# Optimization experiments

Measured on AMD Instinct MI355X. Metric: run time of the kernel, lower is better.

The kernel has to match this reference:

```python
import jax, jax.numpy as jnp
import numpy as np

B, TOPN, OUT, PAD, IOU_TH, IM = 16, 4, 224, 224, 0.25, 448
HP = IM + 2 * PAD  # padded image side = 896

_ANCHOR_SETTINGS = (
    dict(stride=32, size=48, scale=[2 ** (1. / 3.), 2 ** (2. / 3.)], aspect_ratio=[0.667, 1, 1.5]),
    dict(stride=64, size=96, scale=[2 ** (1. / 3.), 2 ** (2. / 3.)], aspect_ratio=[0.667, 1, 1.5]),
    dict(stride=128, size=192, scale=[1, 2 ** (1. / 3.), 2 ** (2. / 3.)], aspect_ratio=[0.667, 1, 1.5]),
)

def _edge_anchors(input_shape=(IM, IM)):
    # NTS-Net generate_default_anchor_maps: per layer, loop scale then aspect,
    # each emitting an HxW map flattened row-major -> matches tidy conv channel-major flatten.
    out = []
    for a in _ANCHOR_SETTINGS:
        st = a['stride']
        H = int(np.ceil(input_shape[0] / st)); W = int(np.ceil(input_shape[1] / st))
        cy = np.broadcast_to((np.arange(H) * st + st / 2.)[:, None], (H, W))
        cx = np.broadcast_to((np.arange(W) * st + st / 2.)[None, :], (H, W))
        for sc in a['scale']:
            for ar in a['aspect_ratio']:
                h = a['size'] * sc / np.sqrt(ar); w = a['size'] * sc * np.sqrt(ar)
                out.append(np.stack([cy - h / 2., cx - w / 2., cy + h / 2., cx + w / 2.], -1).reshape(-1, 4))
    e = np.concatenate(out, 0)
    return (e + PAD).astype(np.int32)  # module does (edge_anchors + 224).astype(int)


def _conv(x, w, b, stride, pad):
    y = jax.lax.conv_general_dilated(x, w, (stride, stride), [(pad, pad), (pad, pad)],
                                     dimension_numbers=('NCHW', 'OIHW', 'NCHW'))
    return y + b[None, :, None, None]


def _proposal_scores(rpn, w1, b1, w2, b2, w3, b3, wt1, bt1, wt2, bt2, wt3, bt3):
    d1 = jax.nn.relu(_conv(rpn, w1, b1, 1, 1))   # [B,128,14,14]
    d2 = jax.nn.relu(_conv(d1, w2, b2, 2, 1))    # [B,128,7,7]
    d3 = jax.nn.relu(_conv(d2, w3, b3, 2, 1))    # [B,128,4,4]
    bsz = rpn.shape[0]
    t1 = _conv(d1, wt1, bt1, 1, 0).reshape(bsz, -1)  # [B,1176]
    t2 = _conv(d2, wt2, bt2, 1, 0).reshape(bsz, -1)  # [B,294]
    t3 = _conv(d3, wt3, bt3, 1, 0).reshape(bsz, -1)  # [B,144]
    return jnp.concatenate([t1, t2, t3], axis=1)     # [B,1614]


def _nms_topn(scores, boxes, areas):
    # greedy hard NMS, fixed TOPN picks, suppress iou >= IOU_TH (matches upstream hard_nms)
    def step(s, _):
        i = jnp.argmax(s)
        sb = boxes[i]
        iy = jnp.clip(jnp.minimum(boxes[:, 2], sb[2]) - jnp.maximum(boxes[:, 0], sb[0]), 0.)
        ix = jnp.clip(jnp.minimum(boxes[:, 3], sb[3]) - jnp.maximum(boxes[:, 1], sb[1]), 0.)
        inter = iy * ix
        iou = inter / (areas + areas[i] - inter)
        return jnp.where(iou >= IOU_TH, -jnp.inf, s), i
    _, idxs = jax.lax.scan(step, scores, None, length=TOPN)
    return idxs  # [TOPN] int


def _crop_resize(x, anchors, top_idx):
    # batched replacement of the per-(i,j) F.interpolate(x_pad[i,:,y0:y1,x0:x1], 224, bilinear, align_corners=True)
    x_pad = jnp.pad(x, ((0, 0), (0, 0), (PAD, PAD), (PAD, PAD)))
    xp = jnp.transpose(x_pad, (0, 2, 3, 1))            # [B,HP,HP,3]
    bxs = anchors[top_idx].astype(jnp.float32)          # [B,T,4] (y0,x0,y1,x1)
    y0, x0, y1, x1 = bxs[..., 0], bxs[..., 1], bxs[..., 2], bxs[..., 3]
    t = jnp.arange(OUT, dtype=jnp.float32) / (OUT - 1)  # align_corners=True grid
    ys = y0[..., None] + t * (y1 - y0 - 1.)[..., None]  # [B,T,S] src rows in padded img
    xs = x0[..., None] + t * (x1 - x0 - 1.)[..., None]
    yi0 = jnp.floor(ys).astype(jnp.int32); yi1 = jnp.minimum(yi0 + 1, HP - 1)
    xi0 = jnp.floor(xs).astype(jnp.int32); xi1 = jnp.minimum(xi0 + 1, HP - 1)
    wy = (ys - yi0)[..., :, None, None]                 # [B,T,S,1,1]
    wx = (xs - xi0)[..., None, :, None]                 # [B,T,1,S,1]
    b = jnp.arange(x.shape[0])[:, None, None, None]
    g = lambda yi, xi: xp[b, yi[..., :, None], xi[..., None, :]]  # [B,T,S,S,3]
    v = (g(yi0, xi0) * (1 - wy) * (1 - wx) + g(yi0, xi1) * (1 - wy) * wx
         + g(yi1, xi0) * wy * (1 - wx) + g(yi1, xi1) * wy * wx)
    return jnp.transpose(v, (0, 1, 4, 2, 3))            # [B,T,3,S,S]


def setup_inputs() -> dict:
    key = jax.random.key(0)
    ks = jax.random.split(key, 16)
    he = lambda k, shape, fan: jax.random.normal(k, shape, jnp.float32) * np.sqrt(2.0 / fan)
    inp = {
        'x': jax.random.normal(ks[0], (B, 3, IM, IM), jnp.float32),
        'rpn_feature': jax.random.uniform(ks[1], (B, 2048, 14, 14), jnp.float32),
        'w_down1': he(ks[2], (128, 2048, 3, 3), 2048 * 9), 'b_down1': jnp.zeros((128,), jnp.float32),
        'w_down2': he(ks[3], (128, 128, 3, 3), 128 * 9),   'b_down2': jnp.zeros((128,), jnp.float32),
        'w_down3': he(ks[4], (128, 128, 3, 3), 128 * 9),   'b_down3': jnp.zeros((128,), jnp.float32),
        'w_tidy1': he(ks[5], (6, 128, 1, 1), 128),         'b_tidy1': jnp.zeros((6,), jnp.float32),
        'w_tidy2': he(ks[6], (6, 128, 1, 1), 128),         'b_tidy2': jnp.zeros((6,), jnp.float32),
        'w_tidy3': he(ks[7], (9, 128, 1, 1), 128),         'b_tidy3': jnp.zeros((9,), jnp.float32),
        'anchors': jnp.asarray(_edge_anchors(), jnp.int32),  # [1614,4]
    }
    return inp


def reference(x, rpn_feature, w_down1, b_down1, w_down2, b_down2, w_down3, b_down3,
              w_tidy1, b_tidy1, w_tidy2, b_tidy2, w_tidy3, b_tidy3, anchors):
    rpn_score = _proposal_scores(rpn_feature, w_down1, b_down1, w_down2, b_down2, w_down3, b_down3,
                                 w_tidy1, b_tidy1, w_tidy2, b_tidy2, w_tidy3, b_tidy3)
    boxes = anchors.astype(jnp.float32)
    areas = (boxes[:, 2] - boxes[:, 0]) * (boxes[:, 3] - boxes[:, 1])
    top_idx = jax.vmap(lambda s: _nms_topn(s, boxes, areas))(rpn_score)       # [B,TOPN]
    top_prob = jnp.take_along_axis(rpn_score, top_idx, axis=1)                # [B,TOPN]
    part_imgs = _crop_resize(x, anchors, top_idx).reshape(B * TOPN, 3, OUT, OUT)
    return part_imgs, top_idx, top_prob, rpn_score
```

## Files before the change

### kernel.cpp

```cpp
#include <hip/hip_runtime.h>
#include <math.h>

#define BATCH 16
#define TOPN 4
#define OUTS 224
#define PADW 224
#define IM 448
#define HP 896
#define NA 1614
#define IC1 2048
#define C128 128

#define N_PART (BATCH*TOPN*3*OUTS*OUTS)
#define OFF_TOPIDX  (N_PART)
#define OFF_TOPPROB (N_PART + BATCH*TOPN)
#define OFF_SCORE   (N_PART + 2*BATCH*TOPN)

#define WS_D1 0
#define WS_IDX (BATCH*C128*196)
#define WS_WT  (WS_IDX + 64)
#define NWT1 (9*2048*128)
#define NWT2 (9*128*128)
#define NIMG (16*32*16384)
#define D1SL 25088

typedef __attribute__((ext_vector_type(8))) short frag8;
typedef __attribute__((ext_vector_type(16))) float acc16;
typedef __attribute__((ext_vector_type(4)))  float acc4;

__device__ __forceinline__ unsigned short f2bf(float f) {
    unsigned int u = __float_as_uint(f);
    u = (u + 0x7fffu + ((u >> 16) & 1u)) >> 16;
    return (unsigned short)u;
}
__device__ __forceinline__ float bf2f(unsigned short h) {
    return __uint_as_float(((unsigned int)h) << 16);
}
__device__ __forceinline__ void cvt4(const float* v, ushort4* h, ushort4* lo) {
    unsigned short hh[4], ll[4];
#pragma unroll
    for (int e = 0; e < 4; ++e) { hh[e] = f2bf(v[e]); ll[e] = f2bf(v[e] - bf2f(hh[e])); }
    *h  = make_ushort4(hh[0], hh[1], hh[2], hh[3]);
    *lo = make_ushort4(ll[0], ll[1], ll[2], ll[3]);
}

__device__ __forceinline__ void w1frag_body(const float* __restrict__ w1,
                                            unsigned short* __restrict__ w1h,
                                            unsigned short* __restrict__ w1l,
                                            int i) {
    if (i >= 32768) return;
    int oc5 = i & 31;
    int q8  = (i >> 5) & 1;
    int ot  = (i >> 6) & 3;
    int c   = (i >> 8) & 3;
    int h   = (i >> 10) & 1;
    int kg  = (i >> 11) & 15;
    int oc  = ot * 32 + oc5;
    int ic0 = kg * 128 + h * 64 + c * 16 + q8 * 8;
    int l   = q8 * 32 + oc5;
    const float* src = w1 + ((size_t)oc * IC1 + ic0) * 9;
    size_t dbase = (size_t)kg * 16384 + h * 8192 + c * 2048 + ot * 512 + l * 8;
#pragma unroll
    for (int t = 0; t < 9; ++t) {
        frag8 hv, lv;
#pragma unroll
        for (int e = 0; e < 8; ++e) {
            float v = src[e * 9 + t];
            unsigned short hs = f2bf(v);
            hv[e] = (short)hs;
            lv[e] = (short)f2bf(v - bf2f(hs));
        }
        size_t dst = dbase + (size_t)t * 262144;
        *(frag8*)&w1h[dst] = hv;
        *(frag8*)&w1l[dst] = lv;
    }
}

__device__ __forceinline__ void wfrag128_body(const float* __restrict__ w,
                                              unsigned short* __restrict__ wh,
                                              unsigned short* __restrict__ wl,
                                              int i) {
    if (i >= 16384) return;
    int oc5 = i & 31;
    int q8  = (i >> 5) & 1;
    int ot  = (i >> 6) & 3;
    int c   = (i >> 8) & 3;
    int h   = (i >> 10) & 1;
    int oc  = ot * 32 + oc5;
    int ic0 = h * 64 + c * 16 + q8 * 8;
    int l   = q8 * 32 + oc5;
    const float* src = w + ((size_t)oc * C128 + ic0) * 9;
    size_t dbase = (size_t)h * 8192 + c * 2048 + ot * 512 + l * 8;
#pragma unroll
    for (int t = 0; t < 9; ++t) {
        frag8 hv, lv;
#pragma unroll
        for (int e = 0; e < 8; ++e) {
            float v = src[e * 9 + t];
            unsigned short hs = f2bf(v);
            hv[e] = (short)hs;
            lv[e] = (short)f2bf(v - bf2f(hs));
        }
        size_t dst = dbase + (size_t)t * 16384;
        *(frag8*)&wh[dst] = hv;
        *(frag8*)&wl[dst] = lv;
    }
}

__global__ __launch_bounds__(256) void k_prep(
    const float* __restrict__ w1, unsigned short* __restrict__ w1h, unsigned short* __restrict__ w1l,
    const float* __restrict__ w2, unsigned short* __restrict__ w2fh, unsigned short* __restrict__ w2fl,
    const float* __restrict__ w3, unsigned short* __restrict__ w3fh, unsigned short* __restrict__ w3fl,
    const float* __restrict__ rpn, unsigned short* __restrict__ imgH) {
    __shared__ float tile[64 * 201];
    const int tid = threadIdx.x;
    const int blk = blockIdx.x;
    if (blk < 128) {
        w1frag_body(w1, w1h, w1l, blk * 256 + tid);
    } else if (blk < 192) {
        wfrag128_body(w2, w2fh, w2fl, (blk - 128) * 256 + tid);
    } else if (blk < 256) {
        wfrag128_body(w3, w3fh, w3fl, (blk - 192) * 256 + tid);
    } else {
        const int bb = blk - 256;
        const int b = bb & 15, icg = bb >> 4;
        const int ic0 = icg * 64;
        char* img = (char*)(imgH + (size_t)bb * 16384);
        for (int qq = tid; qq < 3136; qq += 256) {
            int icl = qq / 49, r = qq % 49, p = r * 4;
            const float4 v = *(const float4*)&rpn[(size_t)(b * IC1 + ic0 + icl) * 196 + p];
            tile[icl * 201 + p + 0] = v.x;
            tile[icl * 201 + p + 1] = v.y;
            tile[icl * 201 + p + 2] = v.z;
            tile[icl * 201 + p + 3] = v.w;
        }
        __syncthreads();
        for (int qq = tid; qq < 3136; qq += 256) {
            int px = qq >> 4, ic4 = (qq & 15) * 4;
            float vv[4];
            unsigned short hh[4];
#pragma unroll
            for (int e = 0; e < 4; ++e) { vv[e] = tile[(ic4 + e) * 201 + px]; hh[e] = f2bf(vv[e]); }
            int pos = (px / 14 + 1) * 16 + (px % 14 + 1);
            int byo = (pos * 128 + ic4 * 2) ^ ((pos & 7) << 4);
            *(ushort4*)(img + byo) = make_ushort4(hh[0], hh[1], hh[2], hh[3]);
        }
        for (int qq = tid; qq < 960; qq += 256) {
            int hp = qq >> 4, sub = qq & 15;
            int pos;
            if (hp < 16)      pos = hp;
            else if (hp < 32) pos = 240 + (hp - 16);
            else if (hp < 46) pos = (hp - 31) * 16;
            else              pos = (hp - 45) * 16 + 15;
            *(ushort4*)(img + pos * 128 + sub * 8) = make_ushort4(0, 0, 0, 0);
        }
    }
}


#define LOADB(it, BH, BL) { \
    const int o_ = ((it) >> 2) * 262144 + ((it) & 3) * 2048; \
    BH = *(const frag8*)&WHb[o_]; BL = *(const frag8*)&WLb[o_]; }

#define DOMFMA(it, BH, BL) { \
    const int tap_ = (it) >> 2; \
    const int off_ = (tap_ / 3) * 16 + (tap_ % 3); \
    const int kb_ = ((it) & 3) * 32 + q * 16; \
    frag8 aH[4]; \
    _Pragma("unroll") \
    for (int mt_ = 0; mt_ < 4; ++mt_) { \
        const int p_ = posa[mt_] + off_; \
        const int by_ = (p_ * 128 + kb_) ^ ((p_ & 7) << 4); \
        aH[mt_] = *(const frag8*)((const char*)inH + by_); \
    } \
    _Pragma("unroll") \
    for (int mt_ = 0; mt_ < 4; ++mt_) { \
        acc[mt_] = __builtin_amdgcn_mfma_f32_32x32x16_bf16(aH[mt_], BH, acc[mt_], 0, 0, 0); \
        acc[mt_] = __builtin_amdgcn_mfma_f32_32x32x16_bf16(aH[mt_], BL, acc[mt_], 0, 0, 0); \
    } }

__global__ __launch_bounds__(512, 4) void k_conv1_mfma(const unsigned short* __restrict__ imgH,
                                                       const unsigned short* __restrict__ wfh,
                                                       const unsigned short* __restrict__ wfl,
                                                       float* __restrict__ d1p) {
    __shared__ unsigned short inH[256 * 64];

    const int tid = threadIdx.x;
    const int blk = blockIdx.x;
    const int b = blk >> 5;
    const int icg = blk & 31;
    const int l = tid & 63, w = tid >> 6;
    const int ln = l & 31, q = l >> 5;
    const int mtw = w & 1, ntw = w >> 1;

    {
        const char* src = (const char*)(imgH + ((size_t)(icg * 16 + b)) * 16384);
        char* dst = (char*)inH;
#pragma unroll
        for (int k = 0; k < 4; ++k) {
            frag8 v = *(const frag8*)(src + tid * 16 + k * 8192);
            *(frag8*)(dst + tid * 16 + k * 8192) = v;
        }
    }

    acc16 acc[4];
#pragma unroll
    for (int mt = 0; mt < 4; ++mt)
#pragma unroll
        for (int r = 0; r < 16; ++r) acc[mt][r] = 0.f;

    int posa[4];
#pragma unroll
    for (int mt = 0; mt < 4; ++mt) {
        int px = mtw * 128 + mt * 32 + ln;
        posa[mt] = (px < 196) ? ((px / 14) * 16 + (px % 14)) : 0;
    }

    const unsigned short* WHb = wfh + (size_t)icg * 8192 + ntw * 512 + (size_t)l * 8;
    const unsigned short* WLb = wfl + (size_t)icg * 8192 + ntw * 512 + (size_t)l * 8;

    __syncthreads();

    frag8 B0H, B0L, B1H, B1L, B2H, B2L;
    LOADB(0, B0H, B0L);
    LOADB(1, B1H, B1L);
    LOADB(2, B2H, B2L);
#pragma unroll
    for (int g = 0; g < 12; ++g) {
        DOMFMA(g * 3 + 0, B0H, B0L); if (g < 11) LOADB(g * 3 + 3, B0H, B0L);
        DOMFMA(g * 3 + 1, B1H, B1L); if (g < 11) LOADB(g * 3 + 4, B1H, B1L);
        DOMFMA(g * 3 + 2, B2H, B2L); if (g < 11) LOADB(g * 3 + 5, B2H, B2L);
    }

    {
        float* out = d1p + (size_t)blk * D1SL;
        const int oc = ntw * 32 + ln;
#pragma unroll
        for (int mt = 0; mt < 4; ++mt) {
#pragma unroll
            for (int r = 0; r < 16; ++r) {
                int m = (r & 3) + 8 * (r >> 2) + 4 * q;
                int px = mtw * 128 + mt * 32 + m;
                if (px < 196)
                    out[px * 128 + oc] = acc[mt][r];
            }
        }
    }
}

__global__ __launch_bounds__(256) void k_reduce(const float* __restrict__ d1p,
                                                const float* __restrict__ b1,
                                                float* __restrict__ d1) {
    int f4 = blockIdx.x * 256 + threadIdx.x;
    int flat = f4 * 4;
    int b = flat / D1SL;
    int inner = flat - b * D1SL;
    const float* src = d1p + (size_t)b * 32 * D1SL + inner;
    float4 s = *(const float4*)&b1[inner & 127];
#pragma unroll 8
    for (int icg = 0; icg < 32; ++icg) {
        float4 v = *(const float4*)&src[(size_t)icg * D1SL];
        s.x += v.x; s.y += v.y; s.z += v.z; s.w += v.w;
    }
    s.x = fmaxf(s.x, 0.f); s.y = fmaxf(s.y, 0.f);
    s.z = fmaxf(s.z, 0.f); s.w = fmaxf(s.w, 0.f);
    *(float4*)&d1[flat] = s;
}


#define LOADB2(it, BH, BL) { \
    const int o_ = ((it) >> 2) * 16384 + ((it) & 3) * 2048; \
    BH = *(const frag8*)&W2H[o_]; BL = *(const frag8*)&W2L[o_]; }

#define DOC2(it, BH, BL) { \
    const int tap_ = (it) >> 2; \
    const int off_ = (tap_ / 3) * 16 + (tap_ % 3); \
    const int ko_ = ((it) & 3) * 16 + q * 8; \
    const int pp_ = (posa2 + off_) * 72 + ko_; \
    frag8 aH = *(const frag8*)&inH[pp_]; \
    frag8 aL = *(const frag8*)&inL[pp_]; \
    c2 = __builtin_amdgcn_mfma_f32_32x32x16_bf16(aH, BH, c2, 0, 0, 0); \
    c2 = __builtin_amdgcn_mfma_f32_32x32x16_bf16(aH, BL, c2, 0, 0, 0); \
    c2 = __builtin_amdgcn_mfma_f32_32x32x16_bf16(aL, BH, c2, 0, 0, 0); }

#define LOADB3(it, BH, BL) { \
    const int o_ = ((it) >> 2) * 16384 + ((it) & 3) * 2048; \
    BH = *(const frag8*)&W3Hp[o_]; BL = *(const frag8*)&W3Lp[o_]; }

#define DOC3(it, BH, BL) { \
    const int tap_ = (it) >> 2; \
    const int off_ = (tap_ / 3) * 16 + (tap_ % 3); \
    const int ko_ = ((it) & 3) * 16 + q * 8; \
    const int pp_ = (posb3 + off_) * 72 + ko_; \
    frag8 aH = *(const frag8*)&dhH[pp_]; \
    frag8 aL = *(const frag8*)&dhL[pp_]; \
    c3 = __builtin_amdgcn_mfma_f32_32x32x16_bf16(aH, BH, c3, 0, 0, 0); \
    c3 = __builtin_amdgcn_mfma_f32_32x32x16_bf16(aH, BL, c3, 0, 0, 0); \
    c3 = __builtin_amdgcn_mfma_f32_32x32x16_bf16(aL, BH, c3, 0, 0, 0); }

__global__ __launch_bounds__(512, 1) void k_tail(
    const float* __restrict__ d1,
    const unsigned short* __restrict__ w2fh, const unsigned short* __restrict__ w2fl,
    const unsigned short* __restrict__ w3fh, const unsigned short* __restrict__ w3fl,
    const float* __restrict__ b2, const float* __restrict__ b3,
    const float* __restrict__ wt1, const float* __restrict__ bt1,
    const float* __restrict__ wt2, const float* __restrict__ bt2,
    const float* __restrict__ wt3, const float* __restrict__ bt3,
    const int* __restrict__ anchors,
    float* __restrict__ score_out, float* __restrict__ out_idx,
    float* __restrict__ out_prob, int* __restrict__ idx_ws) {
    extern __shared__ char smem[];
    unsigned short* inH = (unsigned short*)(smem);
    unsigned short* inL = (unsigned short*)(smem + 43776);
    unsigned short* t1H = (unsigned short*)(smem + 124416);
    unsigned short* t1L = (unsigned short*)(smem + 126720);
    float*  d2f  = (float*)(smem + 129024);
    float*  sbuf = (float*)(smem + 154112);
    unsigned short* dhH = (unsigned short*)(smem);
    unsigned short* dhL = (unsigned short*)(smem + 27648);
    float*  d3f  = (float*)(smem + 55296);
    unsigned short* t2H = (unsigned short*)(smem + 63488);
    unsigned short* t2L = (unsigned short*)(smem + 65792);
    float* wt3s = (float*)(smem);
    float* y0s = (float*)(smem + 6464);
    float* x0s = (float*)(smem + 12928);
    float* y1s = (float*)(smem + 19392);
    float* x1s = (float*)(smem + 25856);
    float* ars = (float*)(smem + 32320);
    float* rv  = (float*)(smem + 38784);
    int*   ri  = (int*)(smem + 39808);

    const int tid = threadIdx.x;
    const int b = blockIdx.x;
    const int l = tid & 63, w = tid >> 6;
    const int ln = l & 31, q = l >> 5;
    const int l16 = l & 15, q4 = l >> 4;

    for (int i = tid; i < 304 * 72; i += 512) { inH[i] = 0; inL[i] = 0; }

    acc16 c2;
    acc4 t1a[2];
#pragma unroll
    for (int r = 0; r < 16; ++r) c2[r] = 0.f;
#pragma unroll
    for (int i = 0; i < 2; ++i)
#pragma unroll
        for (int r = 0; r < 4; ++r) t1a[i][r] = 0.f;

    const int mtw = w & 1, ntw = w >> 1;
    int posa2;
    {
        int px = mtw * 32 + ln;
        posa2 = (px < 49) ? ((px / 7) * 32 + (px % 7) * 2) : 256;
    }
    __syncthreads();

    for (int half = 0; half < 2; ++half) {
        const int ics = half * 64;
        for (int qq = tid; qq < 3136; qq += 512) {
            int px = qq >> 4, ic4 = (qq & 15) * 4;
            float4 v = *(const float4*)&d1[(size_t)(b * 196 + px) * 128 + ics + ic4];
            float vv[4] = {fmaxf(v.x, 0.f), fmaxf(v.y, 0.f), fmaxf(v.z, 0.f), fmaxf(v.w, 0.f)};
            ushort4 h4, l4; cvt4(vv, &h4, &l4);
            int pos = (px / 14 + 1) * 16 + (px % 14 + 1);
            *(ushort4*)&inH[pos * 72 + ic4] = h4;
            *(ushort4*)&inL[pos * 72 + ic4] = l4;
        }
        for (int qq = tid; qq < 1024; qq += 512) {
            int m = qq >> 6, k = qq & 63;
            float v = (m < 6) ? wt1[m * 128 + ics + k] : 0.f;
            unsigned short h = f2bf(v);
            t1H[m * 72 + k] = h;
            t1L[m * 72 + k] = f2bf(v - bf2f(h));
        }
        __syncthreads();

        {
            const unsigned short* W2H = w2fh + half * 8192 + ntw * 512 + (size_t)l * 8;
            const unsigned short* W2L = w2fl + half * 8192 + ntw * 512 + (size_t)l * 8;
            frag8 B0H, B0L, B1H, B1L, B2H, B2L, B3H, B3L;
            LOADB2(0, B0H, B0L);
            LOADB2(1, B1H, B1L);
            LOADB2(2, B2H, B2L);
            LOADB2(3, B3H, B3L);
#pragma unroll
            for (int g = 0; g < 9; ++g) {
                DOC2(g * 4 + 0, B0H, B0L); if (g < 8) LOADB2(g * 4 + 4, B0H, B0L);
                DOC2(g * 4 + 1, B1H, B1L); if (g < 8) LOADB2(g * 4 + 5, B1H, B1L);
                DOC2(g * 4 + 2, B2H, B2L); if (g < 8) LOADB2(g * 4 + 6, B2H, B2L);
                DOC2(g * 4 + 3, B3H, B3L); if (g < 8) LOADB2(g * 4 + 7, B3H, B3L);
            }
        }

#pragma unroll
        for (int i = 0; i < 2; ++i) {
            int px = (w * 2 + i) * 16 + l16;
            int pos = (px < 196) ? ((px / 14 + 1) * 16 + (px % 14 + 1)) : 256;
#pragma unroll
            for (int c = 0; c < 2; ++c) {
                int ko = c * 32 + q4 * 8;
                frag8 aH = *(const frag8*)&t1H[l16 * 72 + ko];
                frag8 aL = *(const frag8*)&t1L[l16 * 72 + ko];
                frag8 bH = *(const frag8*)&inH[pos * 72 + ko];
                frag8 bL = *(const frag8*)&inL[pos * 72 + ko];
                t1a[i] = __builtin_amdgcn_mfma_f32_16x16x32_bf16(aH, bH, t1a[i], 0, 0, 0);
                t1a[i] = __builtin_amdgcn_mfma_f32_16x16x32_bf16(aH, bL, t1a[i], 0, 0, 0);
                t1a[i] = __builtin_amdgcn_mfma_f32_16x16x32_bf16(aL, bH, t1a[i], 0, 0, 0);
            }
        }
        __syncthreads();
    }

    {
        int oc = ntw * 32 + ln;
        float bias = b2[oc];
#pragma unroll
        for (int r = 0; r < 16; ++r) {
            int m = (r & 3) + 8 * (r >> 2) + 4 * q;
            int px = mtw * 32 + m;
            if (px < 49) d2f[px * 128 + oc] = fmaxf(c2[r] + bias, 0.f);
        }
    }
#pragma unroll
    for (int i = 0; i < 2; ++i) {
        int px = (w * 2 + i) * 16 + l16;
#pragma unroll
        for (int r = 0; r < 4; ++r) {
            int oc = q4 * 4 + r;
            if (oc < 6 && px < 196) {
                float v = t1a[i][r] + bt1[oc];
                sbuf[oc * 196 + px] = v;
                score_out[b * NA + oc * 196 + px] = v;
            }
        }
    }
    __syncthreads();

    for (int i = tid; i < 192 * 72; i += 512) { dhH[i] = 0; dhL[i] = 0; }

    acc16 c3;
    acc4 t2a;
#pragma unroll
    for (int r = 0; r < 16; ++r) c3[r] = 0.f;
#pragma unroll
    for (int r = 0; r < 4; ++r) t2a[r] = 0.f;

    const int posb3 = (ln < 16) ? ((ln / 4) * 32 + (ln % 4) * 2) : 144;
    const int pxt2 = (w - 4) * 16 + l16;
    const int posbt2 = (w >= 4 && pxt2 < 49) ? ((pxt2 / 7 + 1) * 16 + (pxt2 % 7 + 1)) : 144;
    __syncthreads();

    for (int half = 0; half < 2; ++half) {
        const int ics = half * 64;
        for (int qq = tid; qq < 784; qq += 512) {
            int px = qq >> 4, ic4 = (qq & 15) * 4;
            float4 v = *(const float4*)&d2f[px * 128 + ics + ic4];
            float vv[4] = {v.x, v.y, v.z, v.w};
            ushort4 h4, l4; cvt4(vv, &h4, &l4);
            int pos = (px / 7 + 1) * 16 + (px % 7 + 1);
            *(ushort4*)&dhH[pos * 72 + ic4] = h4;
            *(ushort4*)&dhL[pos * 72 + ic4] = l4;
        }
        for (int qq = tid; qq < 1024; qq += 512) {
            int m = qq >> 6, k = qq & 63;
            float v = (m < 6) ? wt2[m * 128 + ics + k] : 0.f;
            unsigned short h = f2bf(v);
            t2H[m * 72 + k] = h;
            t2L[m * 72 + k] = f2bf(v - bf2f(h));
        }
        __syncthreads();

        if (w < 4) {
            const unsigned short* W3Hp = w3fh + half * 8192 + w * 512 + (size_t)l * 8;
            const unsigned short* W3Lp = w3fl + half * 8192 + w * 512 + (size_t)l * 8;
            frag8 B0H, B0L, B1H, B1L, B2H, B2L, B3H, B3L;
            LOADB3(0, B0H, B0L);
            LOADB3(1, B1H, B1L);
            LOADB3(2, B2H, B2L);
            LOADB3(3, B3H, B3L);
#pragma unroll
            for (int g = 0; g < 9; ++g) {
                DOC3(g * 4 + 0, B0H, B0L); if (g < 8) LOADB3(g * 4 + 4, B0H, B0L);
                DOC3(g * 4 + 1, B1H, B1L); if (g < 8) LOADB3(g * 4 + 5, B1H, B1L);
                DOC3(g * 4 + 2, B2H, B2L); if (g < 8) LOADB3(g * 4 + 6, B2H, B2L);
                DOC3(g * 4 + 3, B3H, B3L); if (g < 8) LOADB3(g * 4 + 7, B3H, B3L);
            }
        } else {
#pragma unroll
            for (int c = 0; c < 2; ++c) {
                int ko = c * 32 + q4 * 8;
                frag8 aH = *(const frag8*)&t2H[l16 * 72 + ko];
                frag8 aL = *(const frag8*)&t2L[l16 * 72 + ko];
                frag8 bH = *(const frag8*)&dhH[posbt2 * 72 + ko];
                frag8 bL = *(const frag8*)&dhL[posbt2 * 72 + ko];
                t2a = __builtin_amdgcn_mfma_f32_16x16x32_bf16(aH, bH, t2a, 0, 0, 0);
                t2a = __builtin_amdgcn_mfma_f32_16x16x32_bf16(aH, bL, t2a, 0, 0, 0);
                t2a = __builtin_amdgcn_mfma_f32_16x16x32_bf16(aL, bH, t2a, 0, 0, 0);
            }
        }
        __syncthreads();
    }

    if (w < 4) {
        int oc = w * 32 + ln;
        float bias = b3[oc];
#pragma unroll
        for (int r = 0; r < 16; ++r) {
            int px = (r & 3) + 8 * (r >> 2) + 4 * q;
            if (px < 16) d3f[oc * 16 + px] = fmaxf(c3[r] + bias, 0.f);
        }
    } else {
#pragma unroll
        for (int r = 0; r < 4; ++r) {
            int oc = q4 * 4 + r;
            if (oc < 6 && pxt2 < 49) {
                float v = t2a[r] + bt2[oc];
                sbuf[1176 + oc * 49 + pxt2] = v;
                score_out[b * NA + 1176 + oc * 49 + pxt2] = v;
            }
        }
    }
    for (int i = tid; i < 1152; i += 512) wt3s[i] = wt3[i];
    __syncthreads();

    if (tid < 144) {
        int oc = tid >> 4, px = tid & 15;
        float s = bt3[oc];
        for (int ic = 0; ic < 128; ++ic) s += wt3s[oc * 128 + ic] * d3f[ic * 16 + px];
        sbuf[1470 + oc * 16 + px] = s;
        score_out[b * NA + 1470 + oc * 16 + px] = s;
    }
    for (int j = tid; j < NA; j += 512) {
        int4 a = ((const int4*)anchors)[j];
        float a0 = (float)a.x, a1 = (float)a.y, a2 = (float)a.z, a3 = (float)a.w;
        y0s[j] = a0; x0s[j] = a1; y1s[j] = a2; x1s[j] = a3;
        ars[j] = (a2 - a0) * (a3 - a1);
    }
    __syncthreads();

    for (int it = 0; it < TOPN; ++it) {
        float bv = -INFINITY; int bi = NA;
        for (int j = tid; j < NA; j += 512) {
            float v = sbuf[j];
            if (v > bv || (v == bv && j < bi)) { bv = v; bi = j; }
        }
#pragma unroll
        for (int d = 1; d < 64; d <<= 1) {
            float ov = __shfl_xor(bv, d, 64);
            int   oi = __shfl_xor(bi, d, 64);
            if (ov > bv || (ov == bv && oi < bi)) { bv = ov; bi = oi; }
        }
        if (l == 0) { rv[w] = bv; ri[w] = bi; }
        __syncthreads();
        if (tid == 0) {
            float V = rv[0]; int K = ri[0];
#pragma unroll
            for (int j = 1; j < 8; ++j) {
                float ov = rv[j]; int oi = ri[j];
                if (ov > V || (ov == V && oi < K)) { V = ov; K = oi; }
            }
            ri[8] = K;
            out_idx[b * TOPN + it] = (float)K;
            out_prob[b * TOPN + it] = V;
            idx_ws[b * TOPN + it] = K;
        }
        __syncthreads();
        int K = ri[8];
        float ky0 = y0s[K], kx0 = x0s[K], ky1 = y1s[K], kx1 = x1s[K], ka = ars[K];
        for (int j = tid; j < NA; j += 512) {
            float iy = fmaxf(fminf(y1s[j], ky1) - fmaxf(y0s[j], ky0), 0.f);
            float ix = fmaxf(fminf(x1s[j], kx1) - fmaxf(x0s[j], kx0), 0.f);
            float inter = iy * ix;
            float iou = inter / (ars[j] + ka - inter);
            if (iou >= 0.25f) sbuf[j] = -INFINITY;
        }
        __syncthreads();
    }
}

__global__ __launch_bounds__(256) void k_crop(const float* __restrict__ x,
                                              const int* __restrict__ anchors,
                                              const int* __restrict__ idx_ws,
                                              float* __restrict__ out) {
    int blk = blockIdx.x;
    int crop = blk / OUTS;
    int i = blk % OUTS;
    int j = threadIdx.x;
    if (j >= OUTS) return;
    int b = crop >> 2;
    int a = idx_ws[crop];
    int y0 = anchors[a * 4], x0 = anchors[a * 4 + 1];
    int y1 = anchors[a * 4 + 2], x1 = anchors[a * 4 + 3];

    float ti = (float)i / 223.f;
    float ys = (float)y0 + ti * (float)(y1 - y0 - 1);
    int yi0 = (int)ys;
    int yi1 = min(yi0 + 1, HP - 1);
    float wy = ys - (float)yi0;

    float tj = (float)j / 223.f;
    float xs = (float)x0 + tj * (float)(x1 - x0 - 1);
    int xi0 = (int)xs;
    int xi1 = min(xi0 + 1, HP - 1);
    float wx = xs - (float)xi0;

    int ry0 = yi0 - PADW, ry1 = yi1 - PADW, rx0 = xi0 - PADW, rx1 = xi1 - PADW;
    bool vy0 = (ry0 >= 0) && (ry0 < IM), vy1 = (ry1 >= 0) && (ry1 < IM);
    bool vx0 = (rx0 >= 0) && (rx0 < IM), vx1 = (rx1 >= 0) && (rx1 < IM);

    float w00 = (1.f - wy) * (1.f - wx), w01 = (1.f - wy) * wx;
    float w10 = wy * (1.f - wx), w11 = wy * wx;

#pragma unroll
    for (int c = 0; c < 3; ++c) {
        const float* xp = x + (size_t)(b * 3 + c) * IM * IM;
        float g00 = (vy0 && vx0) ? xp[ry0 * IM + rx0] : 0.f;
        float g01 = (vy0 && vx1) ? xp[ry0 * IM + rx1] : 0.f;
        float g10 = (vy1 && vx0) ? xp[ry1 * IM + rx0] : 0.f;
        float g11 = (vy1 && vx1) ? xp[ry1 * IM + rx1] : 0.f;
        out[(size_t)(crop * 3 + c) * OUTS * OUTS + i * OUTS + j] =
            g00 * w00 + g01 * w01 + g10 * w10 + g11 * w11;
    }
}

extern "C" void kernel_launch(void* const* d_in, const int* in_sizes, int n_in,
                              void* d_out, int out_size, void* d_ws, size_t ws_size,
                              hipStream_t stream) {
    (void)in_sizes; (void)n_in; (void)out_size; (void)ws_size;
    const float* x    = (const float*)d_in[0];
    const float* rpn  = (const float*)d_in[1];
    const float* w1   = (const float*)d_in[2];
    const float* b1   = (const float*)d_in[3];
    const float* w2   = (const float*)d_in[4];
    const float* b2   = (const float*)d_in[5];
    const float* w3   = (const float*)d_in[6];
    const float* b3   = (const float*)d_in[7];
    const float* wt1  = (const float*)d_in[8];
    const float* bt1  = (const float*)d_in[9];
    const float* wt2  = (const float*)d_in[10];
    const float* bt2  = (const float*)d_in[11];
    const float* wt3  = (const float*)d_in[12];
    const float* bt3  = (const float*)d_in[13];
    const int*   anc  = (const int*)d_in[14];

    float* out = (float*)d_out;
    float* ws  = (float*)d_ws;
    float* d1  = ws + WS_D1;
    int*   idxw = (int*)(ws + WS_IDX);
    unsigned short* w1h = (unsigned short*)(ws + WS_WT);
    unsigned short* w1l = w1h + NWT1;
    unsigned short* w2fh = w1l + NWT1;
    unsigned short* w2fl = w2fh + NWT2;
    unsigned short* w3fh = w2fl + NWT2;
    unsigned short* w3fl = w3fh + NWT2;
    unsigned short* imgH = w3fl + NWT2;
    float* d1p = (float*)(imgH + NIMG);

    static const int TAIL_LDS = 160568;
    hipFuncSetAttribute((const void*)k_tail, hipFuncAttributeMaxDynamicSharedMemorySize, TAIL_LDS);

    k_prep<<<768, 256, 0, stream>>>(w1, w1h, w1l, w2, w2fh, w2fl, w3, w3fh, w3fl,
                                    rpn, imgH);
    k_conv1_mfma<<<512, 512, 0, stream>>>(imgH, w1h, w1l, d1p);
    k_reduce<<<392, 256, 0, stream>>>(d1p, b1, d1);
    k_tail<<<BATCH, 512, TAIL_LDS, stream>>>(d1, w2fh, w2fl, w3fh, w3fl, b2, b3,
                                             wt1, bt1, wt2, bt2, wt3, bt3, anc,
                                             out + OFF_SCORE, out + OFF_TOPIDX,
                                             out + OFF_TOPPROB, idxw);
    k_crop<<<BATCH * TOPN * OUTS, 256, 0, stream>>>(x, anc, idxw, out);
}
```

Measured before the change: 261.8 us.

## Split tail kernel into conv2, conv3 and NMS kernels with split-K across warps

The single 16-block tail kernel (one block per batch) is split into three kernels. Conv2 and conv3 now run on 128 and 64 blocks that tile over output channels and pixels. Inside each block the four warps split the reduction over channels and combine partial sums through shared memory. Intermediate activations d2/d3 and the scores now go through global memory, and there are two extra kernel launches. The aim is to use far more compute units for the tail, at the cost of the extra global traffic, launch overhead and redundant input staging per block.

```diff
diff --git a/kernel.cpp b/kernel.cpp
--- a/kernel.cpp
+++ b/kernel.cpp
@@ -157,7 +157,6 @@
     }
 }
 
-
 #define LOADB(it, BH, BL) { \
     const int o_ = ((it) >> 2) * 262144 + ((it) & 3) * 2048; \
     BH = *(const frag8*)&WHb[o_]; BL = *(const frag8*)&WLb[o_]; }
@@ -267,77 +266,27 @@
     *(float4*)&d1[flat] = s;
 }
 
-
-#define LOADB2(it, BH, BL) { \
-    const int o_ = ((it) >> 2) * 16384 + ((it) & 3) * 2048; \
-    BH = *(const frag8*)&W2H[o_]; BL = *(const frag8*)&W2L[o_]; }
-
-#define DOC2(it, BH, BL) { \
-    const int tap_ = (it) >> 2; \
-    const int off_ = (tap_ / 3) * 16 + (tap_ % 3); \
-    const int ko_ = ((it) & 3) * 16 + q * 8; \
-    const int pp_ = (posa2 + off_) * 72 + ko_; \
-    frag8 aH = *(const frag8*)&inH[pp_]; \
-    frag8 aL = *(const frag8*)&inL[pp_]; \
-    c2 = __builtin_amdgcn_mfma_f32_32x32x16_bf16(aH, BH, c2, 0, 0, 0); \
-    c2 = __builtin_amdgcn_mfma_f32_32x32x16_bf16(aH, BL, c2, 0, 0, 0); \
-    c2 = __builtin_amdgcn_mfma_f32_32x32x16_bf16(aL, BH, c2, 0, 0, 0); }
-
-#define LOADB3(it, BH, BL) { \
-    const int o_ = ((it) >> 2) * 16384 + ((it) & 3) * 2048; \
-    BH = *(const frag8*)&W3Hp[o_]; BL = *(const frag8*)&W3Lp[o_]; }
-
-#define DOC3(it, BH, BL) { \
-    const int tap_ = (it) >> 2; \
-    const int off_ = (tap_ / 3) * 16 + (tap_ % 3); \
-    const int ko_ = ((it) & 3) * 16 + q * 8; \
-    const int pp_ = (posb3 + off_) * 72 + ko_; \
-    frag8 aH = *(const frag8*)&dhH[pp_]; \
-    frag8 aL = *(const frag8*)&dhL[pp_]; \
-    c3 = __builtin_amdgcn_mfma_f32_32x32x16_bf16(aH, BH, c3, 0, 0, 0); \
-    c3 = __builtin_amdgcn_mfma_f32_32x32x16_bf16(aH, BL, c3, 0, 0, 0); \
-    c3 = __builtin_amdgcn_mfma_f32_32x32x16_bf16(aL, BH, c3, 0, 0, 0); }
-
-__global__ __launch_bounds__(512, 1) void k_tail(
+__global__ __launch_bounds__(256, 1) void k_conv2t1(
     const float* __restrict__ d1,
     const unsigned short* __restrict__ w2fh, const unsigned short* __restrict__ w2fl,
-    const unsigned short* __restrict__ w3fh, const unsigned short* __restrict__ w3fl,
-    const float* __restrict__ b2, const float* __restrict__ b3,
+    const float* __restrict__ b2,
     const float* __restrict__ wt1, const float* __restrict__ bt1,
-    const float* __restrict__ wt2, const float* __restrict__ bt2,
-    const float* __restrict__ wt3, const float* __restrict__ bt3,
-    const int* __restrict__ anchors,
-    float* __restrict__ score_out, float* __restrict__ out_idx,
-    float* __restrict__ out_prob, int* __restrict__ idx_ws) {
-    extern __shared__ char smem[];
-    unsigned short* inH = (unsigned short*)(smem);
-    unsigned short* inL = (unsigned short*)(smem + 43776);
-    unsigned short* t1H = (unsigned short*)(smem + 124416);
-    unsigned short* t1L = (unsigned short*)(smem + 126720);
-    float*  d2f  = (float*)(smem + 129024);
-    float*  sbuf = (float*)(smem + 154112);
-    unsigned short* dhH = (unsigned short*)(smem);
-    unsigned short* dhL = (unsigned short*)(smem + 27648);
-    float*  d3f  = (float*)(smem + 55296);
-    unsigned short* t2H = (unsigned short*)(smem + 63488);
-    unsigned short* t2L = (unsigned short*)(smem + 65792);
-    float* wt3s = (float*)(smem);
-    float* y0s = (float*)(smem + 6464);
-    float* x0s = (float*)(smem + 12928);
-    float* y1s = (float*)(smem + 19392);
-    float* x1s = (float*)(smem + 25856);
-    float* ars = (float*)(smem + 32320);
-    float* rv  = (float*)(smem + 38784);
-    int*   ri  = (int*)(smem + 39808);
+    float* __restrict__ d2, float* __restrict__ score_out) {
+    __shared__ unsigned short inH[304 * 72];
+    __shared__ unsigned short inL[304 * 72];
+    __shared__ unsigned short t1H[16 * 72];
+    __shared__ unsigned short t1L[16 * 72];
+    __shared__ float red[3 * 64 * 16];
 
     const int tid = threadIdx.x;
-    const int b = blockIdx.x;
+    const int blk = blockIdx.x;
+    const int b = blk >> 3;
+    const int pt = (blk >> 2) & 1;
+    const int ot = blk & 3;
     const int l = tid & 63, w = tid >> 6;
     const int ln = l & 31, q = l >> 5;
     const int l16 = l & 15, q4 = l >> 4;
 
-    for (int i = tid; i < 304 * 72; i += 512) { inH[i] = 0; inL[i] = 0; }
-
     acc16 c2;
     acc4 t1a[2];
 #pragma unroll
@@ -347,17 +296,19 @@
 #pragma unroll
         for (int r = 0; r < 4; ++r) t1a[i][r] = 0.f;
 
-    const int mtw = w & 1, ntw = w >> 1;
     int posa2;
     {
-        int px = mtw * 32 + ln;
+        int px = pt * 32 + ln;
         posa2 = (px < 49) ? ((px / 7) * 32 + (px % 7) * 2) : 256;
     }
+    const int ko = w * 16 + q * 8;
+
+    for (int i = tid; i < 304 * 72; i += 256) { inH[i] = 0; inL[i] = 0; }
     __syncthreads();
 
     for (int half = 0; half < 2; ++half) {
         const int ics = half * 64;
-        for (int qq = tid; qq < 3136; qq += 512) {
+        for (int qq = tid; qq < 3136; qq += 256) {
             int px = qq >> 4, ic4 = (qq & 15) * 4;
             float4 v = *(const float4*)&d1[(size_t)(b * 196 + px) * 128 + ics + ic4];
             float vv[4] = {fmaxf(v.x, 0.f), fmaxf(v.y, 0.f), fmaxf(v.z, 0.f), fmaxf(v.w, 0.f)};
@@ -366,77 +317,110 @@
             *(ushort4*)&inH[pos * 72 + ic4] = h4;
             *(ushort4*)&inL[pos * 72 + ic4] = l4;
         }
-        for (int qq = tid; qq < 1024; qq += 512) {
-            int m = qq >> 6, k = qq & 63;
-            float v = (m < 6) ? wt1[m * 128 + ics + k] : 0.f;
-            unsigned short h = f2bf(v);
-            t1H[m * 72 + k] = h;
-            t1L[m * 72 + k] = f2bf(v - bf2f(h));
+        if (ot == 0) {
+            for (int qq = tid; qq < 1024; qq += 256) {
+                int m = qq >> 6, k = qq & 63;
+                float v = (m < 6) ? wt1[m * 128 + ics + k] : 0.f;
+                unsigned short h = f2bf(v);
+                t1H[m * 72 + k] = h;
+                t1L[m * 72 + k] = f2bf(v - bf2f(h));
+            }
         }
         __syncthreads();
 
         {
-            const unsigned short* W2H = w2fh + half * 8192 + ntw * 512 + (size_t)l * 8;
-            const unsigned short* W2L = w2fl + half * 8192 + ntw * 512 + (size_t)l * 8;
-            frag8 B0H, B0L, B1H, B1L, B2H, B2L, B3H, B3L;
-            LOADB2(0, B0H, B0L);
-            LOADB2(1, B1H, B1L);
-            LOADB2(2, B2H, B2L);
-            LOADB2(3, B3H, B3L);
-#pragma unroll
-            for (int g = 0; g < 9; ++g) {
-                DOC2(g * 4 + 0, B0H, B0L); if (g < 8) LOADB2(g * 4 + 4, B0H, B0L);
-                DOC2(g * 4 + 1, B1H, B1L); if (g < 8) LOADB2(g * 4 + 5, B1H, B1L);
-                DOC2(g * 4 + 2, B2H, B2L); if (g < 8) LOADB2(g * 4 + 6, B2H, B2L);
-                DOC2(g * 4 + 3, B3H, B3L); if (g < 8) LOADB2(g * 4 + 7, B3H, B3L);
-            }
-        }
-
+            const unsigned short* W2B  = w2fh + half * 8192 + w * 2048 + ot * 512 + (size_t)l * 8;
+            const unsigned short* W2Bl = w2fl + half * 8192 + w * 2048 + ot * 512 + (size_t)l * 8;
+            frag8 B0H = *(const frag8*)&W2B[0],     B0L = *(const frag8*)&W2Bl[0];
+            frag8 B1H = *(const frag8*)&W2B[16384], B1L = *(const frag8*)&W2Bl[16384];
+#pragma unroll
+            for (int j = 0; j < 9; ++j) {
+                const int off = (j / 3) * 16 + (j % 3);
+                const int pp = (posa2 + off) * 72 + ko;
+                frag8 aH = *(const frag8*)&inH[pp];
+                frag8 aL = *(const frag8*)&inL[pp];
+                frag8 BH = (j & 1) ? B1H : B0H;
+                frag8 BL = (j & 1) ? B1L : B0L;
+                c2 = __builtin_amdgcn_mfma_f32_32x32x16_bf16(aH, BH, c2, 0, 0, 0);
+                c2 = __builtin_amdgcn_mfma_f32_32x32x16_bf16(aH, BL, c2, 0, 0, 0);
+                c2 = __builtin_amdgcn_mfma_f32_32x32x16_bf16(aL, BH, c2, 0, 0, 0);
+                if (j < 7) {
+                    if (j & 1) { B1H = *(const frag8*)&W2B[(j + 2) * 16384]; B1L = *(const frag8*)&W2Bl[(j + 2) * 16384]; }
+                    else       { B0H = *(const frag8*)&W2B[(j + 2) * 16384]; B0L = *(const frag8*)&W2Bl[(j + 2) * 16384]; }
+                }
+            }
+        }
+
+        if (ot == 0) {
+#pragma unroll
+            for (int i = 0; i < 2; ++i) {
+                int px = (pt * 8 + w * 2 + i) * 16 + l16;
+                int pos = (px < 196) ? ((px / 14 + 1) * 16 + (px % 14 + 1)) : 256;
+#pragma unroll
+                for (int c = 0; c < 2; ++c) {
+                    int kot = c * 32 + q4 * 8;
+                    frag8 aH = *(const frag8*)&t1H[l16 * 72 + kot];
+                    frag8 aL = *(const frag8*)&t1L[l16 * 72 + kot];
+                    frag8 bH = *(const frag8*)&inH[pos * 72 + kot];
+                    frag8 bL = *(const frag8*)&inL[pos * 72 + kot];
+                    t1a[i] = __builtin_amdgcn_mfma_f32_16x16x32_bf16(aH, bH, t1a[i], 0, 0, 0);
+                    t1a[i] = __builtin_amdgcn_mfma_f32_16x16x32_bf16(aH, bL, t1a[i], 0, 0, 0);
+                    t1a[i] = __builtin_amdgcn_mfma_f32_16x16x32_bf16(aL, bH, t1a[i], 0, 0, 0);
+                }
+            }
+        }
+        __syncthreads();
+    }
+
+    if (w > 0) {
+#pragma unroll
+        for (int r = 0; r < 16; ++r) red[((w - 1) * 64 + l) * 16 + r] = c2[r];
+    }
+    __syncthreads();
+    if (w == 0) {
+        const int oc = ot * 32 + ln;
+        float bias = b2[oc];
+#pragma unroll
+        for (int r = 0; r < 16; ++r) {
+            float s = c2[r] + red[(0 * 64 + l) * 16 + r] + red[(1 * 64 + l) * 16 + r] + red[(2 * 64 + l) * 16 + r];
+            int m = (r & 3) + 8 * (r >> 2) + 4 * q;
+            int px = pt * 32 + m;
+            if (px < 49) d2[(size_t)(b * 49 + px) * 128 + oc] = fmaxf(s + bias, 0.f);
+        }
+    }
+    if (ot == 0) {
 #pragma unroll
         for (int i = 0; i < 2; ++i) {
-            int px = (w * 2 + i) * 16 + l16;
-            int pos = (px < 196) ? ((px / 14 + 1) * 16 + (px % 14 + 1)) : 256;
-#pragma unroll
-            for (int c = 0; c < 2; ++c) {
-                int ko = c * 32 + q4 * 8;
-                frag8 aH = *(const frag8*)&t1H[l16 * 72 + ko];
-                frag8 aL = *(const frag8*)&t1L[l16 * 72 + ko];
-                frag8 bH = *(const frag8*)&inH[pos * 72 + ko];
-                frag8 bL = *(const frag8*)&inL[pos * 72 + ko];
-                t1a[i] = __builtin_amdgcn_mfma_f32_16x16x32_bf16(aH, bH, t1a[i], 0, 0, 0);
-                t1a[i] = __builtin_amdgcn_mfma_f32_16x16x32_bf16(aH, bL, t1a[i], 0, 0, 0);
-                t1a[i] = __builtin_amdgcn_mfma_f32_16x16x32_bf16(aL, bH, t1a[i], 0, 0, 0);
-            }
-        }
-        __syncthreads();
-    }
-
-    {
-        int oc = ntw * 32 + ln;
-        float bias = b2[oc];
-#pragma unroll
-        for (int r = 0; r < 16; ++r) {
-            int m = (r & 3) + 8 * (r >> 2) + 4 * q;
-            int px = mtw * 32 + m;
-            if (px < 49) d2f[px * 128 + oc] = fmaxf(c2[r] + bias, 0.f);
-        }
-    }
-#pragma unroll
-    for (int i = 0; i < 2; ++i) {
-        int px = (w * 2 + i) * 16 + l16;
-#pragma unroll
-        for (int r = 0; r < 4; ++r) {
-            int oc = q4 * 4 + r;
-            if (oc < 6 && px < 196) {
-                float v = t1a[i][r] + bt1[oc];
-                sbuf[oc * 196 + px] = v;
-                score_out[b * NA + oc * 196 + px] = v;
-            }
-        }
-    }
-    __syncthreads();
-
-    for (int i = tid; i < 192 * 72; i += 512) { dhH[i] = 0; dhL[i] = 0; }
+            int px = (pt * 8 + w * 2 + i) * 16 + l16;
+#pragma unroll
+            for (int r = 0; r < 4; ++r) {
+                int oc = q4 * 4 + r;
+                if (oc < 6 && px < 196)
+                    score_out[b * NA + oc * 196 + px] = t1a[i][r] + bt1[oc];
+            }
+        }
+    }
+}
+
+__global__ __launch_bounds__(256, 1) void k_conv3t2(
+    const float* __restrict__ d2,
+    const unsigned short* __restrict__ w3fh, const unsigned short* __restrict__ w3fl,
+    const float* __restrict__ b3,
+    const float* __restrict__ wt2, const float* __restrict__ bt2,
+    float* __restrict__ d3, float* __restrict__ score_out) {
+    __shared__ unsigned short dhH[192 * 72];
+    __shared__ unsigned short dhL[192 * 72];
+    __shared__ unsigned short t2H[16 * 72];
+    __shared__ unsigned short t2L[16 * 72];
+    __shared__ float red[3 * 64 * 16];
+
+    const int tid = threadIdx.x;
+    const int blk = blockIdx.x;
+    const int b = blk >> 2;
+    const int ot = blk & 3;
+    const int l = tid & 63, w = tid >> 6;
+    const int ln = l & 31, q = l >> 5;
+    const int l16 = l & 15, q4 = l >> 4;
 
     acc16 c3;
     acc4 t2a;
@@ -446,53 +430,66 @@
     for (int r = 0; r < 4; ++r) t2a[r] = 0.f;
 
     const int posb3 = (ln < 16) ? ((ln / 4) * 32 + (ln % 4) * 2) : 144;
-    const int pxt2 = (w - 4) * 16 + l16;
-    const int posbt2 = (w >= 4 && pxt2 < 49) ? ((pxt2 / 7 + 1) * 16 + (pxt2 % 7 + 1)) : 144;
+    const int pxt2 = w * 16 + l16;
+    const int posbt2 = (pxt2 < 49) ? ((pxt2 / 7 + 1) * 16 + (pxt2 % 7 + 1)) : 144;
+    const int ko = w * 16 + q * 8;
+
+    for (int i = tid; i < 192 * 72; i += 256) { dhH[i] = 0; dhL[i] = 0; }
     __syncthreads();
 
     for (int half = 0; half < 2; ++half) {
         const int ics = half * 64;
-        for (int qq = tid; qq < 784; qq += 512) {
+        for (int qq = tid; qq < 784; qq += 256) {
             int px = qq >> 4, ic4 = (qq & 15) * 4;
-            float4 v = *(const float4*)&d2f[px * 128 + ics + ic4];
+            float4 v = *(const float4*)&d2[(size_t)(b * 49 + px) * 128 + ics + ic4];
             float vv[4] = {v.x, v.y, v.z, v.w};
             ushort4 h4, l4; cvt4(vv, &h4, &l4);
             int pos = (px / 7 + 1) * 16 + (px % 7 + 1);
             *(ushort4*)&dhH[pos * 72 + ic4] = h4;
             *(ushort4*)&dhL[pos * 72 + ic4] = l4;
         }
-        for (int qq = tid; qq < 1024; qq += 512) {
-            int m = qq >> 6, k = qq & 63;
-            float v = (m < 6) ? wt2[m * 128 + ics + k] : 0.f;
-            unsigned short h = f2bf(v);
-            t2H[m * 72 + k] = h;
-            t2L[m * 72 + k] = f2bf(v - bf2f(h));
-        }
-        __syncthreads();
-
-        if (w < 4) {
-            const unsigned short* W3Hp = w3fh + half * 8192 + w * 512 + (size_t)l * 8;
-            const unsigned short* W3Lp = w3fl + half * 8192 + w * 512 + (size_t)l * 8;
-            frag8 B0H, B0L, B1H, B1L, B2H, B2L, B3H, B3L;
-            LOADB3(0, B0H, B0L);
-            LOADB3(1, B1H, B1L);
-            LOADB3(2, B2H, B2L);
-            LOADB3(3, B3H, B3L);
-#pragma unroll
-            for (int g = 0; g < 9; ++g) {
-                DOC3(g * 4 + 0, B0H, B0L); if (g < 8) LOADB3(g * 4 + 4, B0H, B0L);
-                DOC3(g * 4 + 1, B1H, B1L); if (g < 8) LOADB3(g * 4 + 5, B1H, B1L);
-                DOC3(g * 4 + 2, B2H, B2L); if (g < 8) LOADB3(g * 4 + 6, B2H, B2L);
-                DOC3(g * 4 + 3, B3H, B3L); if (g < 8) LOADB3(g * 4 + 7, B3H, B3L);
-            }
-        } else {
+        if (ot == 0) {
+            for (int qq = tid; qq < 1024; qq += 256) {
+                int m = qq >> 6, k = qq & 63;
+                float v = (m < 6) ? wt2[m * 128 + ics + k] : 0.f;
+                unsigned short h = f2bf(v);
+                t2H[m * 72 + k] = h;
+                t2L[m * 72 + k] = f2bf(v - bf2f(h));
+            }
+        }
+        __syncthreads();
+
+        {
+            const unsigned short* W3B  = w3fh + half * 8192 + w * 2048 + ot * 512 + (size_t)l * 8;
+            const unsigned short* W3Bl = w3fl + half * 8192 + w * 2048 + ot * 512 + (size_t)l * 8;
+            frag8 B0H = *(const frag8*)&W3B[0],     B0L = *(const frag8*)&W3Bl[0];
+            frag8 B1H = *(const frag8*)&W3B[16384], B1L = *(const frag8*)&W3Bl[16384];
+#pragma unroll
+            for (int j = 0; j < 9; ++j) {
+                const int off = (j / 3) * 16 + (j % 3);
+                const int pp = (posb3 + off) * 72 + ko;
+                frag8 aH = *(const frag8*)&dhH[pp];
+                frag8 aL = *(const frag8*)&dhL[pp];
+                frag8 BH = (j & 1) ? B1H : B0H;
+                frag8 BL = (j & 1) ? B1L : B0L;
+                c3 = __builtin_amdgcn_mfma_f32_32x32x16_bf16(aH, BH, c3, 0, 0, 0);
+                c3 = __builtin_amdgcn_mfma_f32_32x32x16_bf16(aH, BL, c3, 0, 0, 0);
+                c3 = __builtin_amdgcn_mfma_f32_32x32x16_bf16(aL, BH, c3, 0, 0, 0);
+                if (j < 7) {
+                    if (j & 1) { B1H = *(const frag8*)&W3B[(j + 2) * 16384]; B1L = *(const frag8*)&W3Bl[(j + 2) * 16384]; }
+                    else       { B0H = *(const frag8*)&W3B[(j + 2) * 16384]; B0L = *(const frag8*)&W3Bl[(j + 2) * 16384]; }
+                }
+            }
+        }
+
+        if (ot == 0) {
 #pragma unroll
             for (int c = 0; c < 2; ++c) {
-                int ko = c * 32 + q4 * 8;
-                frag8 aH = *(const frag8*)&t2H[l16 * 72 + ko];
-                frag8 aL = *(const frag8*)&t2L[l16 * 72 + ko];
-                frag8 bH = *(const frag8*)&dhH[posbt2 * 72 + ko];
-                frag8 bL = *(const frag8*)&dhL[posbt2 * 72 + ko];
+                int kot = c * 32 + q4 * 8;
+                frag8 aH = *(const frag8*)&t2H[l16 * 72 + kot];
+                frag8 aL = *(const frag8*)&t2L[l16 * 72 + kot];
+                frag8 bH = *(const frag8*)&dhH[posbt2 * 72 + kot];
+                frag8 bL = *(const frag8*)&dhL[posbt2 * 72 + kot];
                 t2a = __builtin_amdgcn_mfma_f32_16x16x32_bf16(aH, bH, t2a, 0, 0, 0);
                 t2a = __builtin_amdgcn_mfma_f32_16x16x32_bf16(aH, bL, t2a, 0, 0, 0);
                 t2a = __builtin_amdgcn_mfma_f32_16x16x32_bf16(aL, bH, t2a, 0, 0, 0);
@@ -501,40 +498,63 @@
         __syncthreads();
     }
 
-    if (w < 4) {
-        int oc = w * 32 + ln;
+    if (w > 0) {
+#pragma unroll
+        for (int r = 0; r < 16; ++r) red[((w - 1) * 64 + l) * 16 + r] = c3[r];
+    }
+    __syncthreads();
+    if (w == 0) {
+        const int oc = ot * 32 + ln;
         float bias = b3[oc];
 #pragma unroll
         for (int r = 0; r < 16; ++r) {
+            float s = c3[r] + red[(0 * 64 + l) * 16 + r] + red[(1 * 64 + l) * 16 + r] + red[(2 * 64 + l) * 16 + r];
             int px = (r & 3) + 8 * (r >> 2) + 4 * q;
-            if (px < 16) d3f[oc * 16 + px] = fmaxf(c3[r] + bias, 0.f);
-        }
-    } else {
+            if (px < 16) d3[(size_t)(b * 128 + oc) * 16 + px] = fmaxf(s + bias, 0.f);
+        }
+    }
+    if (ot == 0) {
 #pragma unroll
         for (int r = 0; r < 4; ++r) {
             int oc = q4 * 4 + r;
-            if (oc < 6 && pxt2 < 49) {
-                float v = t2a[r] + bt2[oc];
-                sbuf[1176 + oc * 49 + pxt2] = v;
-                score_out[b * NA + 1176 + oc * 49 + pxt2] = v;
-            }
-        }
-    }
+            if (oc < 6 && pxt2 < 49)
+                score_out[b * NA + 1176 + oc * 49 + pxt2] = t2a[r] + bt2[oc];
+        }
+    }
+}
+
+__global__ __launch_bounds__(512, 1) void k_t3nms(
+    const float* __restrict__ d3, const float* __restrict__ wt3, const float* __restrict__ bt3,
+    const int* __restrict__ anchors, float* __restrict__ score_out,
+    float* __restrict__ out_idx, float* __restrict__ out_prob, int* __restrict__ idx_ws) {
+    __shared__ float wt3s[1152];
+    __shared__ float d3s[2048];
+    __shared__ float sbuf[NA];
+    __shared__ float y0s[NA], x0s[NA], y1s[NA], x1s[NA], ars[NA];
+    __shared__ float rv[8];
+    __shared__ int ri[9];
+
+    const int tid = threadIdx.x;
+    const int b = blockIdx.x;
+    const int l = tid & 63, w = tid >> 6;
+
     for (int i = tid; i < 1152; i += 512) wt3s[i] = wt3[i];
-    __syncthreads();
-
-    if (tid < 144) {
-        int oc = tid >> 4, px = tid & 15;
-        float s = bt3[oc];
-        for (int ic = 0; ic < 128; ++ic) s += wt3s[oc * 128 + ic] * d3f[ic * 16 + px];
-        sbuf[1470 + oc * 16 + px] = s;
-        score_out[b * NA + 1470 + oc * 16 + px] = s;
-    }
+    for (int i = tid; i < 2048; i += 512) d3s[i] = d3[b * 2048 + i];
+    for (int j = tid; j < 1470; j += 512) sbuf[j] = score_out[b * NA + j];
     for (int j = tid; j < NA; j += 512) {
         int4 a = ((const int4*)anchors)[j];
         float a0 = (float)a.x, a1 = (float)a.y, a2 = (float)a.z, a3 = (float)a.w;
         y0s[j] = a0; x0s[j] = a1; y1s[j] = a2; x1s[j] = a3;
         ars[j] = (a2 - a0) * (a3 - a1);
+    }
+    __syncthreads();
+
+    if (tid < 144) {
+        int oc = tid >> 4, px = tid & 15;
+        float s = bt3[oc];
+        for (int ic = 0; ic < 128; ++ic) s += wt3s[oc * 128 + ic] * d3s[ic * 16 + px];
+        sbuf[1470 + oc * 16 + px] = s;
+        score_out[b * NA + 1470 + oc * 16 + px] = s;
     }
     __syncthreads();
 
@@ -655,17 +675,18 @@
     unsigned short* w3fl = w3fh + NWT2;
     unsigned short* imgH = w3fl + NWT2;
     float* d1p = (float*)(imgH + NIMG);
-
-    static const int TAIL_LDS = 160568;
-    hipFuncSetAttribute((const void*)k_tail, hipFuncAttributeMaxDynamicSharedMemorySize, TAIL_LDS);
+    float* d2  = d1p + (size_t)512 * D1SL;
+    float* d3  = d2 + 16 * 49 * 128;
 
     k_prep<<<768, 256, 0, stream>>>(w1, w1h, w1l, w2, w2fh, w2fl, w3, w3fh, w3fl,
                                     rpn, imgH);
     k_conv1_mfma<<<512, 512, 0, stream>>>(imgH, w1h, w1l, d1p);
     k_reduce<<<392, 256, 0, stream>>>(d1p, b1, d1);
-    k_tail<<<BATCH, 512, TAIL_LDS, stream>>>(d1, w2fh, w2fl, w3fh, w3fl, b2, b3,
-                                             wt1, bt1, wt2, bt2, wt3, bt3, anc,
-                                             out + OFF_SCORE, out + OFF_TOPIDX,
-                                             out + OFF_TOPPROB, idxw);
+    k_conv2t1<<<128, 256, 0, stream>>>(d1, w2fh, w2fl, b2, wt1, bt1,
+                                       d2, out + OFF_SCORE);
+    k_conv3t2<<<64, 256, 0, stream>>>(d2, w3fh, w3fl, b3, wt2, bt2,
+                                      d3, out + OFF_SCORE);
+    k_t3nms<<<BATCH, 512, 0, stream>>>(d3, wt3, bt3, anc, out + OFF_SCORE,
+                                       out + OFF_TOPIDX, out + OFF_TOPPROB, idxw);
     k_crop<<<BATCH * TOPN * OUTS, 256, 0, stream>>>(x, anc, idxw, out);
 }
```

Result: no change. 257.6 us (-1.6%).
